# Kernel tuning notes

Measured on AMD Instinct MI355X. Metric: run time of the kernel, lower is better.

Reference implementation:

```python
import jax, jax.numpy as jnp
import numpy as np

TOKENS = 8192
MODEL_DIM = 4096
NUM_EXPERTS = 64
K = 2


def setup_inputs() -> dict:
    key = jax.random.key(0)
    kx, kw = jax.random.split(key)
    x = jax.random.normal(kx, (TOKENS, MODEL_DIM), dtype=jnp.float32)
    # nn.Linear default init: U(-1/sqrt(fan_in), 1/sqrt(fan_in)); weight shape [E, D]
    bound = 1.0 / np.sqrt(MODEL_DIM)
    W = jax.random.uniform(kw, (NUM_EXPERTS, MODEL_DIM), dtype=jnp.float32,
                           minval=-bound, maxval=bound)
    return {"x": x, "W": W}


def reference(x, W):
    # TopKGate.forward with k=2, eval mode (no noise): logits -> top2gating
    logits = jnp.einsum("td,ed->te", x.astype(jnp.float32), W)  # [T, E]
    # topk indices (sorted by value, like torch.topk)
    _, topi = jax.lax.top_k(logits, K)                           # [T, K]
    gates = jax.nn.softmax(logits, axis=-1)                      # [T, E]
    # (gates * one_hot(idx)).sum(-1) == gather of gates at idx
    g = jnp.take_along_axis(gates, topi, axis=-1)                # [T, K]
    eps = jnp.finfo(gates.dtype).eps
    denom = jnp.maximum(jnp.sum(g, axis=-1, keepdims=True), eps)
    g = g / denom
    # matches return ([idx1, idx2], [gate1, gate2]) with flattened indices
    return (topi[:, 0], topi[:, 1], g[:, 0], g[:, 1])
```

## Files before the change

kernel.cpp:

```cpp
#include <hip/hip_runtime.h>
#include <float.h>
#include <math.h>

#define TOKENS 8192
#define DIM    4096

typedef _Float16 v8h  __attribute__((ext_vector_type(8)));
typedef float    v4f  __attribute__((ext_vector_type(4)));

__global__ __launch_bounds__(256) void prep_w_kernel(
    const float* __restrict__ W, _Float16* __restrict__ WF) {
    int n = blockIdx.x * 256 + threadIdx.x;
    int chunk = n >> 8;
    int et    = (n >> 6) & 3;
    int lane  = n & 63;
    int e  = et * 16 + (lane & 15);
    int k0 = chunk * 32 + (lane >> 4) * 8;
    const float* src = W + (size_t)e * DIM + k0;
    v8h h, l;
    #pragma unroll
    for (int j = 0; j < 8; ++j) {
        float w = src[j];
        _Float16 wh = (_Float16)w;
        h[j] = wh;
        l[j] = (_Float16)((w - (float)wh) * 2048.0f);
    }
    size_t base = (size_t)chunk * 4096 + (size_t)et * 512 + (size_t)lane * 8;
    *(v8h*)(WF + base)        = h;
    *(v8h*)(WF + base + 2048) = l;
}

#define LOAD_A(Aa, Ab, cc) do {                                               \
    const float* ap_ = abase + (cc) * 32;                                     \
    Aa = *(const float4*)ap_;                                                 \
    Ab = *(const float4*)(ap_ + 4);                                           \
} while (0)

#define LOAD_BH(H0, H1, L0, L1, cc, half) do {                                \
    const _Float16* hp_ = wbH + (size_t)(cc) * 4096 + (half) * 1024;          \
    const _Float16* lp_ = wbL + (size_t)(cc) * 4096 + (half) * 1024;          \
    H0 = *(const v8h*)(hp_);                                                  \
    H1 = *(const v8h*)(hp_ + 512);                                            \
    L0 = *(const v8h*)(lp_);                                                  \
    L1 = *(const v8h*)(lp_ + 512);                                            \
} while (0)

#define CVT1(f, j) {                                                          \
    _Float16 h_ = (_Float16)(f);                                              \
    ah[j] = h_;                                                               \
    al[j] = (_Float16)(((f) - (float)h_) * 2048.0f);                          \
}
#define CVT(Aa, Ab) do {                                                      \
    CVT1(Aa.x, 0) CVT1(Aa.y, 1) CVT1(Aa.z, 2) CVT1(Aa.w, 3)                   \
    CVT1(Ab.x, 4) CVT1(Ab.y, 5) CVT1(Ab.z, 6) CVT1(Ab.w, 7)                   \
} while (0)

#define COMP_HALF(e0, H0, H1, L0, L1) do {                                    \
    acc1[e0]     = __builtin_amdgcn_mfma_f32_16x16x32_f16(ah, H0, acc1[e0], 0, 0, 0);     \
    acc1[e0 + 1] = __builtin_amdgcn_mfma_f32_16x16x32_f16(ah, H1, acc1[e0 + 1], 0, 0, 0); \
    acc2[e0]     = __builtin_amdgcn_mfma_f32_16x16x32_f16(al, H0, acc2[e0], 0, 0, 0);     \
    acc2[e0]     = __builtin_amdgcn_mfma_f32_16x16x32_f16(ah, L0, acc2[e0], 0, 0, 0);     \
    acc2[e0 + 1] = __builtin_amdgcn_mfma_f32_16x16x32_f16(al, H1, acc2[e0 + 1], 0, 0, 0); \
    acc2[e0 + 1] = __builtin_amdgcn_mfma_f32_16x16x32_f16(ah, L1, acc2[e0 + 1], 0, 0, 0); \
} while (0)

#define CHUNK_FULL(AXa, AXb, cc) do {                                         \
    CVT(AXa, AXb);                                                            \
    COMP_HALF(0, B0a, B0b, B0c, B0d);                                         \
    LOAD_BH(B0a, B0b, B0c, B0d, (cc) + 1, 0);                                 \
    COMP_HALF(2, B1a, B1b, B1c, B1d);                                         \
    LOAD_BH(B1a, B1b, B1c, B1d, (cc) + 1, 1);                                 \
    __builtin_amdgcn_sched_barrier(0);                                        \
    LOAD_A(AXa, AXb, (cc) + 4);                                               \
} while (0)

#define CHUNK_NB(AXa, AXb, cc) do {                  \
    CVT(AXa, AXb);                                                            \
    COMP_HALF(0, B0a, B0b, B0c, B0d);                                         \
    LOAD_BH(B0a, B0b, B0c, B0d, (cc) + 1, 0);                                 \
    COMP_HALF(2, B1a, B1b, B1c, B1d);                                         \
    LOAD_BH(B1a, B1b, B1c, B1d, (cc) + 1, 1);                                 \
} while (0)

#define CHUNK_LAST(AXa, AXb) do {                         \
    CVT(AXa, AXb);                                                            \
    COMP_HALF(0, B0a, B0b, B0c, B0d);                                         \
    COMP_HALF(2, B1a, B1b, B1c, B1d);                                         \
} while (0)

__global__ __launch_bounds__(512, 4) void topkgate_kernel(
    const float* __restrict__ x,
    const _Float16* __restrict__ WF,
    float* __restrict__ out) {

    __shared__ float red[8][16][65];

    const int tid  = threadIdx.x;
    const int wq   = tid >> 6;
    const int lane = tid & 63;
    const int tok0 = blockIdx.x * 16;
    const int art  = lane & 15;
    const int akg  = lane >> 4;
    const int chunk0 = wq * 16;

    const float*    abase = x   + (size_t)(tok0 + art) * DIM + chunk0 * 32 + akg * 8;
    const _Float16* wbH   = WF  + (size_t)chunk0 * 4096 + (size_t)lane * 8;
    const _Float16* wbL   = wbH + 2048;

    v4f acc1[4], acc2[4];
    #pragma unroll
    for (int e4 = 0; e4 < 4; ++e4) { acc1[e4] = (v4f)0.0f; acc2[e4] = (v4f)0.0f; }

    float4 A0a, A0b, A1a, A1b, A2a, A2b, A3a, A3b;
    v8h B0a, B0b, B0c, B0d, B1a, B1b, B1c, B1d;
    v8h ah, al;

    LOAD_BH(B0a, B0b, B0c, B0d, 0, 0);
    LOAD_BH(B1a, B1b, B1c, B1d, 0, 1);
    LOAD_A(A0a, A0b, 0);
    LOAD_A(A1a, A1b, 1);
    LOAD_A(A2a, A2b, 2);
    LOAD_A(A3a, A3b, 3);

    #pragma unroll 1
    for (int c = 0; c < 12; c += 4) {
        CHUNK_FULL(A0a, A0b, c);
        CHUNK_FULL(A1a, A1b, c + 1);
        CHUNK_FULL(A2a, A2b, c + 2);
        CHUNK_FULL(A3a, A3b, c + 3);
    }
    CHUNK_NB(A0a, A0b, 12);
    CHUNK_NB(A1a, A1b, 13);
    CHUNK_NB(A2a, A2b, 14);
    CHUNK_LAST(A3a, A3b);

    const float inv2048 = 1.0f / 2048.0f;
    #pragma unroll
    for (int e4 = 0; e4 < 4; ++e4) {
        #pragma unroll
        for (int r = 0; r < 4; ++r) {
            red[wq][akg * 4 + r][e4 * 16 + art] = acc1[e4][r] + acc2[e4][r] * inv2048;
        }
    }
    __syncthreads();

    #pragma unroll
    for (int tt = 0; tt < 2; ++tt) {
        int t = wq * 2 + tt;
        float v = red[0][t][lane] + red[1][t][lane]
                + red[2][t][lane] + red[3][t][lane]
                + red[4][t][lane] + red[5][t][lane]
                + red[6][t][lane] + red[7][t][lane];

        float bv = v; int bi = lane;
        #pragma unroll
        for (int off = 32; off >= 1; off >>= 1) {
            float ov = __shfl_xor(bv, off);
            int   oi = __shfl_xor(bi, off);
            if (ov > bv || (ov == bv && oi < bi)) { bv = ov; bi = oi; }
        }
        float v2 = (lane == bi) ? -FLT_MAX : v;
        float bv2 = v2; int bi2 = lane;
        #pragma unroll
        for (int off = 32; off >= 1; off >>= 1) {
            float ov = __shfl_xor(bv2, off);
            int   oi = __shfl_xor(bi2, off);
            if (ov > bv2 || (ov == bv2 && oi < bi2)) { bv2 = ov; bi2 = oi; }
        }

        if (lane == 0) {
            float g0 = 1.0f / (1.0f + expf(bv2 - bv));
            int gt = tok0 + t;
            out[gt]              = (float)bi;
            out[TOKENS + gt]     = (float)bi2;
            out[2 * TOKENS + gt] = g0;
            out[3 * TOKENS + gt] = 1.0f - g0;
        }
    }
}

extern "C" void kernel_launch(void* const* d_in, const int* in_sizes, int n_in,
                              void* d_out, int out_size, void* d_ws, size_t ws_size,
                              hipStream_t stream) {
    const float* x = (const float*)d_in[0];
    const float* W = (const float*)d_in[1];
    float* out     = (float*)d_out;
    _Float16* WF   = (_Float16*)d_ws;

    prep_w_kernel<<<128, 256, 0, stream>>>(W, WF);
    topkgate_kernel<<<TOKENS / 16, 512, 0, stream>>>(x, WF, out);
}
```

Baseline: 46.43 us.

## Share W tiles across 128-token blocks via LDS async staging and split-K reduction

The fused kernel, where each block of 16 tokens split K across 8 waves and every wave loaded its own W slice into registers, is replaced. A logits kernel now gives each block 128 tokens (8 waves of 16) over one of 8 K-groups, and stages the shared W chunk into double-buffered LDS with global_load_lds so all waves reuse it. The per-K-group partial logits go to a workspace buffer, and a second kernel sums them and does the top-2 and softmax. This cuts repeated W traffic, but it adds an extra kernel launch, a partial-sum round trip through global memory (8x8192x64 floats), and a block barrier on every chunk.

```diff
diff --git a/kernel.cpp b/kernel.cpp
--- a/kernel.cpp
+++ b/kernel.cpp
@@ -7,6 +7,13 @@
 
 typedef _Float16 v8h  __attribute__((ext_vector_type(8)));
 typedef float    v4f  __attribute__((ext_vector_type(4)));
+
+typedef __attribute__((address_space(3))) unsigned int lds_uint;
+typedef const __attribute__((address_space(1))) unsigned int glob_uint;
+
+__device__ __forceinline__ void stage16(const _Float16* g, _Float16* l) {
+    __builtin_amdgcn_global_load_lds((glob_uint*)g, (lds_uint*)l, 16, 0, 0);
+}
 
 __global__ __launch_bounds__(256) void prep_w_kernel(
     const float* __restrict__ W, _Float16* __restrict__ WF) {
@@ -36,14 +43,7 @@
     Ab = *(const float4*)(ap_ + 4);                                           \
 } while (0)
 
-#define LOAD_BH(H0, H1, L0, L1, cc, half) do {                                \
-    const _Float16* hp_ = wbH + (size_t)(cc) * 4096 + (half) * 1024;          \
-    const _Float16* lp_ = wbL + (size_t)(cc) * 4096 + (half) * 1024;          \
-    H0 = *(const v8h*)(hp_);                                                  \
-    H1 = *(const v8h*)(hp_ + 512);                                            \
-    L0 = *(const v8h*)(lp_);                                                  \
-    L1 = *(const v8h*)(lp_ + 512);                                            \
-} while (0)
+#define STAGE(BI, cc) stage16(sbase + (size_t)(cc) * 4096, &buf[BI][wq * 512])
 
 #define CVT1(f, j) {                                                          \
     _Float16 h_ = (_Float16)(f);                                              \
@@ -55,102 +55,121 @@
     CVT1(Ab.x, 4) CVT1(Ab.y, 5) CVT1(Ab.z, 6) CVT1(Ab.w, 7)                   \
 } while (0)
 
-#define COMP_HALF(e0, H0, H1, L0, L1) do {                                    \
-    acc1[e0]     = __builtin_amdgcn_mfma_f32_16x16x32_f16(ah, H0, acc1[e0], 0, 0, 0);     \
-    acc1[e0 + 1] = __builtin_amdgcn_mfma_f32_16x16x32_f16(ah, H1, acc1[e0 + 1], 0, 0, 0); \
-    acc2[e0]     = __builtin_amdgcn_mfma_f32_16x16x32_f16(al, H0, acc2[e0], 0, 0, 0);     \
-    acc2[e0]     = __builtin_amdgcn_mfma_f32_16x16x32_f16(ah, L0, acc2[e0], 0, 0, 0);     \
-    acc2[e0 + 1] = __builtin_amdgcn_mfma_f32_16x16x32_f16(al, H1, acc2[e0 + 1], 0, 0, 0); \
-    acc2[e0 + 1] = __builtin_amdgcn_mfma_f32_16x16x32_f16(ah, L1, acc2[e0 + 1], 0, 0, 0); \
-} while (0)
-
-#define CHUNK_FULL(AXa, AXb, cc) do {                                         \
-    CVT(AXa, AXb);                                                            \
-    COMP_HALF(0, B0a, B0b, B0c, B0d);                                         \
-    LOAD_BH(B0a, B0b, B0c, B0d, (cc) + 1, 0);                                 \
-    COMP_HALF(2, B1a, B1b, B1c, B1d);                                         \
-    LOAD_BH(B1a, B1b, B1c, B1d, (cc) + 1, 1);                                 \
+#define MFMA16(a, b, c) __builtin_amdgcn_mfma_f32_16x16x32_f16(a, b, c, 0, 0, 0)
+
+#define COMPC(BI, Aa, Ab) do {                                                \
+    CVT(Aa, Ab);                                                              \
+    const _Float16* bp_ = &buf[BI][0] + (size_t)lane * 8;                     \
+    v8h h0_ = *(const v8h*)(bp_);                                             \
+    v8h h1_ = *(const v8h*)(bp_ + 512);                                       \
+    v8h h2_ = *(const v8h*)(bp_ + 1024);                                      \
+    v8h h3_ = *(const v8h*)(bp_ + 1536);                                      \
+    v8h l0_ = *(const v8h*)(bp_ + 2048);                                      \
+    v8h l1_ = *(const v8h*)(bp_ + 2560);                                      \
+    v8h l2_ = *(const v8h*)(bp_ + 3072);                                      \
+    v8h l3_ = *(const v8h*)(bp_ + 3584);                                      \
+    acc1[0] = MFMA16(ah, h0_, acc1[0]);                                       \
+    acc1[1] = MFMA16(ah, h1_, acc1[1]);                                       \
+    acc1[2] = MFMA16(ah, h2_, acc1[2]);                                       \
+    acc1[3] = MFMA16(ah, h3_, acc1[3]);                                       \
+    acc2[0] = MFMA16(al, h0_, acc2[0]);  acc2[0] = MFMA16(ah, l0_, acc2[0]);  \
+    acc2[1] = MFMA16(al, h1_, acc2[1]);  acc2[1] = MFMA16(ah, l1_, acc2[1]);  \
+    acc2[2] = MFMA16(al, h2_, acc2[2]);  acc2[2] = MFMA16(ah, l2_, acc2[2]);  \
+    acc2[3] = MFMA16(al, h3_, acc2[3]);  acc2[3] = MFMA16(ah, l3_, acc2[3]);  \
+} while (0)
+
+#define BARRIER_KEEP(n) do {                                                  \
     __builtin_amdgcn_sched_barrier(0);                                        \
-    LOAD_A(AXa, AXb, (cc) + 4);                                               \
-} while (0)
-
-#define CHUNK_NB(AXa, AXb, cc) do {                  \
-    CVT(AXa, AXb);                                                            \
-    COMP_HALF(0, B0a, B0b, B0c, B0d);                                         \
-    LOAD_BH(B0a, B0b, B0c, B0d, (cc) + 1, 0);                                 \
-    COMP_HALF(2, B1a, B1b, B1c, B1d);                                         \
-    LOAD_BH(B1a, B1b, B1c, B1d, (cc) + 1, 1);                                 \
-} while (0)
-
-#define CHUNK_LAST(AXa, AXb) do {                         \
-    CVT(AXa, AXb);                                                            \
-    COMP_HALF(0, B0a, B0b, B0c, B0d);                                         \
-    COMP_HALF(2, B1a, B1b, B1c, B1d);                                         \
-} while (0)
-
-__global__ __launch_bounds__(512, 4) void topkgate_kernel(
+    asm volatile("s_waitcnt vmcnt(" #n ")" ::: "memory");                     \
+    __builtin_amdgcn_sched_barrier(0);                                        \
+    __builtin_amdgcn_s_barrier();                                             \
+    __builtin_amdgcn_sched_barrier(0);                                        \
+} while (0)
+
+#define ITER_FULL(c, ACa, ACb, ALa, ALb, BCUR, BNXT) do {                     \
+    STAGE(BNXT, (c) + 1);                                                     \
+    LOAD_A(ALa, ALb, (c) + 2);                                                \
+    COMPC(BCUR, ACa, ACb);                                                    \
+    BARRIER_KEEP(2);                                                          \
+} while (0)
+
+#define ITER_STAGE_ONLY(c, ACa, ACb, BCUR, BNXT) do {                         \
+    STAGE(BNXT, (c) + 1);                                                     \
+    COMPC(BCUR, ACa, ACb);                                                    \
+    BARRIER_KEEP(0);                                                          \
+} while (0)
+
+__global__ __launch_bounds__(512, 4) void logits_kernel(
     const float* __restrict__ x,
     const _Float16* __restrict__ WF,
-    float* __restrict__ out) {
-
-    __shared__ float red[8][16][65];
+    float* __restrict__ P) {
+
+    __shared__ _Float16 buf[2][4096];
 
     const int tid  = threadIdx.x;
     const int wq   = tid >> 6;
     const int lane = tid & 63;
-    const int tok0 = blockIdx.x * 16;
+    const int kg   = (int)(blockIdx.x & 7);
+    const int tg   = (int)(blockIdx.x >> 3);
+    const int tok0 = tg * 128 + wq * 16;
     const int art  = lane & 15;
     const int akg  = lane >> 4;
-    const int chunk0 = wq * 16;
-
-    const float*    abase = x   + (size_t)(tok0 + art) * DIM + chunk0 * 32 + akg * 8;
-    const _Float16* wbH   = WF  + (size_t)chunk0 * 4096 + (size_t)lane * 8;
-    const _Float16* wbL   = wbH + 2048;
+    const int chunk0 = kg * 16;
+
+    const float*    abase = x  + (size_t)(tok0 + art) * DIM + chunk0 * 32 + akg * 8;
+    const _Float16* sbase = WF + (size_t)chunk0 * 4096 + (size_t)tid * 8;
 
     v4f acc1[4], acc2[4];
     #pragma unroll
     for (int e4 = 0; e4 < 4; ++e4) { acc1[e4] = (v4f)0.0f; acc2[e4] = (v4f)0.0f; }
 
-    float4 A0a, A0b, A1a, A1b, A2a, A2b, A3a, A3b;
-    v8h B0a, B0b, B0c, B0d, B1a, B1b, B1c, B1d;
+    float4 A0a, A0b, A1a, A1b, A2a, A2b;
     v8h ah, al;
 
-    LOAD_BH(B0a, B0b, B0c, B0d, 0, 0);
-    LOAD_BH(B1a, B1b, B1c, B1d, 0, 1);
+    STAGE(0, 0);
     LOAD_A(A0a, A0b, 0);
     LOAD_A(A1a, A1b, 1);
-    LOAD_A(A2a, A2b, 2);
-    LOAD_A(A3a, A3b, 3);
-
-    #pragma unroll 1
-    for (int c = 0; c < 12; c += 4) {
-        CHUNK_FULL(A0a, A0b, c);
-        CHUNK_FULL(A1a, A1b, c + 1);
-        CHUNK_FULL(A2a, A2b, c + 2);
-        CHUNK_FULL(A3a, A3b, c + 3);
+    BARRIER_KEEP(4);
+
+    ITER_FULL(0,  A0a, A0b, A2a, A2b, 0, 1);
+    ITER_FULL(1,  A1a, A1b, A0a, A0b, 1, 0);
+    ITER_FULL(2,  A2a, A2b, A1a, A1b, 0, 1);
+    ITER_FULL(3,  A0a, A0b, A2a, A2b, 1, 0);
+    ITER_FULL(4,  A1a, A1b, A0a, A0b, 0, 1);
+    ITER_FULL(5,  A2a, A2b, A1a, A1b, 1, 0);
+    ITER_FULL(6,  A0a, A0b, A2a, A2b, 0, 1);
+    ITER_FULL(7,  A1a, A1b, A0a, A0b, 1, 0);
+    ITER_FULL(8,  A2a, A2b, A1a, A1b, 0, 1);
+    ITER_FULL(9,  A0a, A0b, A2a, A2b, 1, 0);
+    ITER_FULL(10, A1a, A1b, A0a, A0b, 0, 1);
+    ITER_FULL(11, A2a, A2b, A1a, A1b, 1, 0);
+    ITER_FULL(12, A0a, A0b, A2a, A2b, 0, 1);
+    ITER_FULL(13, A1a, A1b, A0a, A0b, 1, 0);
+    ITER_STAGE_ONLY(14, A2a, A2b, 0, 1);
+    COMPC(1, A0a, A0b);
+
+    const float inv2048 = 1.0f / 2048.0f;
+    #pragma unroll
+    for (int e4 = 0; e4 < 4; ++e4) {
+        #pragma unroll
+        for (int r = 0; r < 4; ++r) {
+            float v = acc1[e4][r] + acc2[e4][r] * inv2048;
+            P[((size_t)kg * TOKENS + tok0 + akg * 4 + r) * 64 + e4 * 16 + art] = v;
+        }
     }
-    CHUNK_NB(A0a, A0b, 12);
-    CHUNK_NB(A1a, A1b, 13);
-    CHUNK_NB(A2a, A2b, 14);
-    CHUNK_LAST(A3a, A3b);
-
-    const float inv2048 = 1.0f / 2048.0f;
-    #pragma unroll
-    for (int e4 = 0; e4 < 4; ++e4) {
-        #pragma unroll
-        for (int r = 0; r < 4; ++r) {
-            red[wq][akg * 4 + r][e4 * 16 + art] = acc1[e4][r] + acc2[e4][r] * inv2048;
-        }
-    }
-    __syncthreads();
-
-    #pragma unroll
-    for (int tt = 0; tt < 2; ++tt) {
-        int t = wq * 2 + tt;
-        float v = red[0][t][lane] + red[1][t][lane]
-                + red[2][t][lane] + red[3][t][lane]
-                + red[4][t][lane] + red[5][t][lane]
-                + red[6][t][lane] + red[7][t][lane];
+}
+
+__global__ __launch_bounds__(256) void reduce_topk_kernel(
+    const float* __restrict__ P, float* __restrict__ out) {
+    const int wq   = threadIdx.x >> 6;
+    const int lane = threadIdx.x & 63;
+    #pragma unroll
+    for (int tt = 0; tt < 4; ++tt) {
+        int gt = blockIdx.x * 16 + wq * 4 + tt;
+        float v = 0.f;
+        #pragma unroll
+        for (int kg = 0; kg < 8; ++kg)
+            v += P[((size_t)kg * TOKENS + gt) * 64 + lane];
 
         float bv = v; int bi = lane;
         #pragma unroll
@@ -170,7 +189,6 @@
 
         if (lane == 0) {
             float g0 = 1.0f / (1.0f + expf(bv2 - bv));
-            int gt = tok0 + t;
             out[gt]              = (float)bi;
             out[TOKENS + gt]     = (float)bi2;
             out[2 * TOKENS + gt] = g0;
@@ -186,7 +204,9 @@
     const float* W = (const float*)d_in[1];
     float* out     = (float*)d_out;
     _Float16* WF   = (_Float16*)d_ws;
+    float* P       = (float*)((char*)d_ws + (1 << 20));
 
     prep_w_kernel<<<128, 256, 0, stream>>>(W, WF);
-    topkgate_kernel<<<TOKENS / 16, 512, 0, stream>>>(x, WF, out);
-}
+    logits_kernel<<<512, 512, 0, stream>>>(x, WF, P);
+    reduce_topk_kernel<<<512, 256, 0, stream>>>(P, out);
+}
```

New measurement: 41.08 us. -11.5%, faster.
